# Performance work log

Hardware: AMD Instinct MI355X
Metric: run time of the kernel (lower is better)

Reference implementation:

```python
import jax, jax.numpy as jnp
import numpy as np

NR, NL, K, TOPK, C, B = 4096, 16384, 8, 10, 16, 4
W_OCC, W_MDN, W_INT = 0.2, 1.0, 0.1
LOG2PI = float(np.log(2.0 * np.pi))


def setup_inputs() -> dict:
    key = jax.random.key(0)
    ks = jax.random.split(key, 12)
    radar_indices = jnp.concatenate([
        jax.random.randint(ks[0], (NR, 1), 0, B),
        jax.random.randint(ks[1], (NR, 1), 0, 41),
        jax.random.randint(ks[2], (NR, 2), 0, 176),
    ], axis=1).astype(jnp.int32)
    lidar_indices = jnp.concatenate([
        jax.random.randint(ks[3], (NL, 1), 0, B),
        jax.random.randint(ks[4], (NL, 1), 0, 41),
        jax.random.randint(ks[5], (NL, 2), 0, 176),
    ], axis=1).astype(jnp.int32)
    return {
        'mu_off': jax.random.normal(ks[6], (NR, K, 3)) * 2.0,
        'log_sig_off': jax.random.normal(ks[7], (NR, K, 3)) * 0.3,
        'mu_int': jax.random.normal(ks[8], (NR, K, 1)),
        'occ_logit': jax.random.normal(ks[9], (NR, K, 1)),
        'mix_logit': jax.random.normal(ks[10], (NR, K, 1)),
        'lidar_features': jax.random.normal(ks[11], (NL, C)),
        'radar_indices': radar_indices,
        'lidar_indices': lidar_indices,
        'gt_topk': TOPK,
    }


def _match(radar_indices, lidar_indices, topk):
    # per-batch top-k nearest lidar voxels for each radar voxel (vectorized:
    # dense masked distance matrix replaces the per-batch python loop)
    rb, lb = radar_indices[:, 0], lidar_indices[:, 0]
    rpos = radar_indices[:, 1:].astype(jnp.float32)  # (Nr,3) zyx
    lpos = lidar_indices[:, 1:].astype(jnp.float32)  # (Nl,3)
    d2 = ((rpos * rpos).sum(-1)[:, None] + (lpos * lpos).sum(-1)[None, :]
          - 2.0 * (rpos @ lpos.T))  # (Nr,Nl) squared dist, same order as cdist
    same = rb[:, None] == lb[None, :]
    d2 = jnp.where(same, d2, jnp.inf)  # cross-batch pairs excluded
    _, nn_idx = jax.lax.top_k(-d2, topk)  # (Nr,topk) smallest distances
    matched = same.any(axis=1)  # (Nr,)
    offs_zyx = (lidar_indices[nn_idx, 1:]
                - radar_indices[:, None, 1:]).astype(jnp.float32)  # (Nr,topk,3)
    offs_zyx = jnp.where(matched[:, None, None], offs_zyx, 0.0)
    return matched, nn_idx, offs_zyx


def reference(mu_off, log_sig_off, mu_int, occ_logit, mix_logit,
              lidar_features, radar_indices, lidar_indices, gt_topk):
    matched, nn_idx, offs_zyx = _match(radar_indices, lidar_indices, gt_topk)
    gt_feat = jnp.where(matched[:, None, None], lidar_features[nn_idx], 0.0)  # (Nr,T,C)
    y = offs_zyx[..., ::-1]  # flip zyx -> xyz, (Nr,T,3)

    # occupancy BCE-with-logits against matched mask
    occ_any = occ_logit[..., 0].max(axis=1)  # (Nr,)
    tgt = matched.astype(occ_any.dtype)
    occ_loss = (tgt * jax.nn.softplus(-occ_any)
                + (1.0 - tgt) * jax.nn.softplus(occ_any)).mean()

    # MDN log-prob: (Nr,T,K) mixture components
    log_pi = jax.nn.log_softmax(mix_logit[..., 0], axis=1)  # (Nr,K)
    mu_ = mu_off[:, None, :, :]       # (Nr,1,K,3)
    ls_ = log_sig_off[:, None, :, :]
    sigma2 = jnp.exp(2.0 * ls_) + 1e-12
    y_ = y[:, :, None, :]             # (Nr,T,1,3)
    logN = -0.5 * (((y_ - mu_) ** 2) / sigma2 + 2.0 * ls_ + LOG2PI).sum(-1)  # (Nr,T,K)
    log_post = logN + log_pi[:, None, :]
    logp = jax.nn.logsumexp(log_post, axis=-1)  # (Nr,T)

    # masked means emulate boolean-index-then-mean over matched rows
    m = matched.astype(jnp.float32)
    cnt = m.sum()
    T = logp.shape[1]
    mdn_nll = -(logp * m[:, None]).sum() / (cnt * T)

    # intensity loss (C % 4 == 0 path)
    gt_int = gt_feat.reshape(gt_feat.shape[0], gt_feat.shape[1], C // 4, 4)[..., 3].mean(axis=2)  # (Nr,T)
    r = jax.nn.softmax(log_post, axis=-1)  # (Nr,T,K) responsibilities
    term = r * jnp.abs(mu_int[:, None, :, 0] - gt_int[:, :, None])  # (Nr,T,K)
    int_loss = (term * m[:, None, None]).sum() / (cnt * T * r.shape[-1])

    return W_OCC * occ_loss + W_MDN * mdn_nll + W_INT * int_loss
```

## Files before the change

kernel.cpp:

```cpp
#include <hip/hip_runtime.h>
#include <cstdint>

#define NRAD 4096
#define NLID 16384
#define KMIX 8
#define TOPK 10
#define CF   16
#define NBIN 176
#define LOG2PI 1.8378770664093453f

static constexpr unsigned INF_D2 = 62851u;

__device__ __forceinline__ void insert_key(unsigned (&t)[TOPK], unsigned key) {
#pragma unroll
    for (int i = TOPK - 1; i >= 1; --i) {
        unsigned hi = key > t[i - 1] ? key : t[i - 1];
        t[i] = hi < t[i] ? hi : t[i];
    }
    t[0] = key < t[0] ? key : t[0];
}

__device__ __forceinline__ void merge10(unsigned (&t)[TOPK], int lane,
                                        unsigned& mine, unsigned& first, unsigned& tenth) {
#pragma unroll
    for (int r = 0; r < TOPK; ++r) {
        unsigned v = t[0];
#pragma unroll
        for (int off = 32; off >= 1; off >>= 1) {
            unsigned o = __shfl_xor(v, off, 64);
            v = o < v ? o : v;
        }
        if (t[0] == v) {
#pragma unroll
            for (int i = 0; i < TOPK - 1; ++i) t[i] = t[i + 1];
            t[TOPK - 1] = 0xFFFFFFFFu;
        }
        if (lane == r) mine = v;
        if (r == 0) first = v;
        if (r == TOPK - 1) tenth = v;
    }
}

__device__ __forceinline__ float waveReduceSum(float v) {
#pragma unroll
    for (int off = 32; off >= 1; off >>= 1) v += __shfl_down(v, off, 64);
    return v;
}

__device__ __forceinline__ void scan_range(unsigned (&t)[TOPK], const uint2* __restrict__ base,
                                           int s, int e, int rz, int ry, int rx, int lane) {
    for (int i = s + lane; i < e; i += 64) {
        uint2 c = base[i];
        int dz = (int)((c.x >> 16) & 63u)  - rz;
        int dy = (int)((c.x >> 8)  & 255u) - ry;
        int dx = (int)(c.x & 255u)         - rx;
        unsigned d2 = (unsigned)(__mul24(dz, dz) + __mul24(dy, dy) + __mul24(dx, dx));
        unsigned key = (d2 << 14) | c.y;
        if (key < t[TOPK - 1]) insert_key(t, key);
    }
}

__global__ __launch_bounds__(1024) void prep_kernel(
        const int* __restrict__ lidar_indices,
        unsigned* __restrict__ packed_full,
        uint2* __restrict__ compacted,
        int* __restrict__ binoff_g,
        int* __restrict__ ctrl) {
    __shared__ int hist[NBIN];
    __shared__ int binoff_s[NBIN + 1];
    __shared__ int bcur[NBIN];
    int tid = threadIdx.x, myb = blockIdx.x;
    if (tid < NBIN) hist[tid] = 0;

    int4 li[NLID / 1024];
#pragma unroll
    for (int it = 0; it < NLID / 1024; ++it)
        li[it] = ((const int4*)lidar_indices)[it * 1024 + tid];
    __syncthreads();

#pragma unroll
    for (int it = 0; it < NLID / 1024; ++it)
        if (li[it].x == myb) atomicAdd(&hist[li[it].z], 1);
    __syncthreads();

    if (tid <= NBIN) {
        int s = 0;
        for (int j = 0; j < tid; ++j) s += hist[j];
        binoff_s[tid] = s;
    }
    __syncthreads();
    if (tid < NBIN) bcur[tid] = binoff_s[tid];
    __syncthreads();

#pragma unroll
    for (int it = 0; it < NLID / 1024; ++it) {
        int i = it * 1024 + tid;
        unsigned pos = ((unsigned)li[it].y << 16) | ((unsigned)li[it].z << 8) | (unsigned)li[it].w;
        if (li[it].x == myb) {
            packed_full[i] = ((unsigned)li[it].x << 22) | pos;
            int dst = atomicAdd(&bcur[li[it].z], 1);
            compacted[myb * NLID + dst] = make_uint2(pos, (unsigned)i);
        }
    }

    __syncthreads();
    if (tid <= NBIN) binoff_g[myb * (NBIN + 1) + tid] = binoff_s[tid];
    if (tid == 0)    ctrl[myb] = binoff_s[NBIN];
    if (myb == 0 && tid >= 64 && tid < 69) ctrl[4 + (tid - 64)] = 0;
}

__global__ __launch_bounds__(256) void topk_kernel(
        const uint2* __restrict__ compacted,
        const unsigned* __restrict__ packed_full,
        const int* __restrict__ ctrl,
        const int* __restrict__ binoff_g,
        const int* __restrict__ radar_indices,
        int* __restrict__ nn_out, int* __restrict__ matched_out) {
    int lane = threadIdx.x & 63;
    int row  = blockIdx.x * 4 + (threadIdx.x >> 6);
    int4 ri = ((const int4*)radar_indices)[row];
    int rb = ri.x, rz = ri.y, ry = ri.z, rx = ri.w;
    const int* boff = binoff_g + rb * (NBIN + 1);

    int lo = ry - 16; lo = lo < 0 ? 0 : lo;
    int hi = ry + 17; hi = hi > NBIN ? NBIN : hi;
    int s = boff[lo], e = boff[hi];

    unsigned t[TOPK];
#pragma unroll
    for (int i = 0; i < TOPK; ++i) t[i] = 0xFFFFFFFFu;

    const uint2* base = compacted + rb * NLID;
    scan_range(t, base, s, e, rz, ry, rx, lane);

    unsigned mine = 0xFFFFFFFFu, first = 0, tenth = 0;
    merge10(t, lane, mine, first, tenth);
    bool matched = true;

    unsigned lim = 0xFFFFFFFFu;
    if (lo > 0)    { unsigned d = (unsigned)(ry - lo + 1); unsigned v = d * d; lim = v < lim ? v : lim; }
    if (hi < NBIN) { unsigned d = (unsigned)(hi - ry);     unsigned v = d * d; lim = v < lim ? v : lim; }

    if ((tenth >> 14) >= lim) {
#pragma unroll
        for (int i = 0; i < TOPK; ++i) t[i] = 0xFFFFFFFFu;
        t[0] = mine;
        scan_range(t, base, boff[0], s, rz, ry, rx, lane);
        scan_range(t, base, e, boff[NBIN], rz, ry, rx, lane);
        merge10(t, lane, mine, first, tenth);
    }

    if (tenth == 0xFFFFFFFFu) {
#pragma unroll
        for (int i = 0; i < TOPK; ++i) t[i] = 0xFFFFFFFFu;
        for (int it = 0; it < NLID / 256; ++it) {
            uint4 p4 = ((const uint4*)packed_full)[it * 64 + lane];
            unsigned bse = it * 256 + lane * 4;
            unsigned ps[4] = {p4.x, p4.y, p4.z, p4.w};
#pragma unroll
            for (int j = 0; j < 4; ++j) {
                unsigned p = ps[j];
                int b  = (int)(p >> 22);
                int dz = (int)((p >> 16) & 63u)  - rz;
                int dy = (int)((p >> 8)  & 255u) - ry;
                int dx = (int)(p & 255u)         - rx;
                unsigned d2 = (unsigned)(__mul24(dz, dz) + __mul24(dy, dy) + __mul24(dx, dx));
                unsigned hi2 = (b == rb) ? d2 : INF_D2;
                insert_key(t, (hi2 << 14) | (bse + j));
            }
        }
        merge10(t, lane, mine, first, tenth);
        matched = first < (INF_D2 << 14);
    }

    if (lane < TOPK) nn_out[row * TOPK + lane] = (int)(mine & 0x3FFFu);
    if (lane == 0)   matched_out[row] = matched ? 1 : 0;
}

__global__ __launch_bounds__(256) void mdn_kernel(
        const float* __restrict__ mu_off, const float* __restrict__ log_sig_off,
        const float* __restrict__ mu_int, const float* __restrict__ occ_logit,
        const float* __restrict__ mix_logit, const float* __restrict__ lidar_features,
        const int* __restrict__ radar_indices, const int* __restrict__ lidar_indices,
        const int* __restrict__ nn, const int* __restrict__ matched,
        float* __restrict__ accum,
        unsigned* __restrict__ dctr,
        float* __restrict__ out) {
    int gid = blockIdx.x * 256 + threadIdx.x;
    int n  = gid / TOPK;
    int tt = gid - n * TOPK;
    int m  = matched[n];
    float mf = (float)m;
    int nni = nn[gid];

    int4 ri = ((const int4*)radar_indices)[n];
    int4 li = ((const int4*)lidar_indices)[nni];
    float y0 = mf * (float)(li.w - ri.w);
    float y1 = mf * (float)(li.z - ri.z);
    float y2 = mf * (float)(li.y - ri.y);

    float mix[KMIX];
    float mmax = -1e30f;
#pragma unroll
    for (int k = 0; k < KMIX; ++k) {
        mix[k] = mix_logit[n * KMIX + k];
        mmax = fmaxf(mmax, mix[k]);
    }
    float msum = 0.f;
#pragma unroll
    for (int k = 0; k < KMIX; ++k) msum += expf(mix[k] - mmax);
    float logZ = mmax + logf(msum);

    float lpost[KMIX];
    float pmax = -1e30f;
#pragma unroll
    for (int k = 0; k < KMIX; ++k) {
        int bidx = (n * KMIX + k) * 3;
        float mu0 = mu_off[bidx + 0], mu1 = mu_off[bidx + 1], mu2 = mu_off[bidx + 2];
        float l0 = log_sig_off[bidx + 0], l1 = log_sig_off[bidx + 1], l2 = log_sig_off[bidx + 2];
        float s0 = expf(2.f * l0) + 1e-12f;
        float s1 = expf(2.f * l1) + 1e-12f;
        float s2 = expf(2.f * l2) + 1e-12f;
        float d0 = y0 - mu0, d1 = y1 - mu1, d2v = y2 - mu2;
        float q = d0 * d0 / s0 + d1 * d1 / s1 + d2v * d2v / s2
                + 2.f * (l0 + l1 + l2) + 3.f * LOG2PI;
        lpost[k] = -0.5f * q + (mix[k] - logZ);
        pmax = fmaxf(pmax, lpost[k]);
    }
    float ex[KMIX];
    float se = 0.f;
#pragma unroll
    for (int k = 0; k < KMIX; ++k) { ex[k] = expf(lpost[k] - pmax); se += ex[k]; }
    float logp = pmax + logf(se);

    float gt = 0.f;
    if (m) {
        const float* lf = lidar_features + nni * CF;
        gt = 0.25f * (lf[3] + lf[7] + lf[11] + lf[15]);
    }
    float inv_se = 1.f / se;
    float isum = 0.f;
#pragma unroll
    for (int k = 0; k < KMIX; ++k)
        isum += ex[k] * inv_se * fabsf(mu_int[n * KMIX + k] - gt);

    float lp = mf * logp;
    float ip = mf * isum;
    float oc = 0.f, mc = 0.f;
    if (tt == 0) {
        float oa = -1e30f;
#pragma unroll
        for (int k = 0; k < KMIX; ++k) oa = fmaxf(oa, occ_logit[n * KMIX + k]);
        float soft_abs = log1pf(expf(-fabsf(oa)));
        oc = mf * (soft_abs + fmaxf(-oa, 0.f)) + (1.f - mf) * (soft_abs + fmaxf(oa, 0.f));
        mc = mf;
    }

    lp = waveReduceSum(lp); ip = waveReduceSum(ip);
    oc = waveReduceSum(oc); mc = waveReduceSum(mc);
    __shared__ float sA[4], sB[4], sC[4], sD[4];
    int wid = threadIdx.x >> 6, lane = threadIdx.x & 63;
    if (lane == 0) { sA[wid] = lp; sB[wid] = ip; sC[wid] = oc; sD[wid] = mc; }
    __syncthreads();
    if (threadIdx.x == 0) {
        atomicAdd(&accum[0], sA[0] + sA[1] + sA[2] + sA[3]);
        atomicAdd(&accum[1], sB[0] + sB[1] + sB[2] + sB[3]);
        atomicAdd(&accum[2], sC[0] + sC[1] + sC[2] + sC[3]);
        atomicAdd(&accum[3], sD[0] + sD[1] + sD[2] + sD[3]);
        __threadfence();
        unsigned done = atomicAdd(dctr, 1u);
        if (done == gridDim.x - 1) {
            __threadfence();
            float a = __hip_atomic_load(&accum[0], __ATOMIC_RELAXED, __HIP_MEMORY_SCOPE_AGENT);
            float b = __hip_atomic_load(&accum[1], __ATOMIC_RELAXED, __HIP_MEMORY_SCOPE_AGENT);
            float c = __hip_atomic_load(&accum[2], __ATOMIC_RELAXED, __HIP_MEMORY_SCOPE_AGENT);
            float d = __hip_atomic_load(&accum[3], __ATOMIC_RELAXED, __HIP_MEMORY_SCOPE_AGENT);
            float occ_loss = c / (float)NRAD;
            float mdn_nll  = -a / (d * (float)TOPK);
            float int_loss = b / (d * (float)TOPK * (float)KMIX);
            out[0] = 0.2f * occ_loss + mdn_nll + 0.1f * int_loss;
        }
    }
}

extern "C" void kernel_launch(void* const* d_in, const int* in_sizes, int n_in,
                              void* d_out, int out_size, void* d_ws, size_t ws_size,
                              hipStream_t stream) {
    const float* mu_off         = (const float*)d_in[0];
    const float* log_sig_off    = (const float*)d_in[1];
    const float* mu_int         = (const float*)d_in[2];
    const float* occ_logit      = (const float*)d_in[3];
    const float* mix_logit      = (const float*)d_in[4];
    const float* lidar_features = (const float*)d_in[5];
    const int*   radar_indices  = (const int*)d_in[6];
    const int*   lidar_indices  = (const int*)d_in[7];
    float* out = (float*)d_out;

    char* ws = (char*)d_ws;
    unsigned* packed_full = (unsigned*)(ws + 0);
    uint2*    compacted   = (uint2*)(ws + 65536);
    int*      ctrl        = (int*)(ws + 589824);
    int*      nn          = (int*)(ws + 589888);
    int*      matched     = (int*)(ws + 753728);
    int*      binoff_g    = (int*)(ws + 770112);

    float*    accum = (float*)(ctrl + 4);
    unsigned* dctr  = (unsigned*)(ctrl + 8);

    hipLaunchKernelGGL(prep_kernel, dim3(4), dim3(1024), 0, stream,
                       lidar_indices, packed_full, compacted, binoff_g, ctrl);
    hipLaunchKernelGGL(topk_kernel, dim3(NRAD / 4), dim3(256), 0, stream,
                       compacted, packed_full, ctrl, binoff_g, radar_indices, nn, matched);
    hipLaunchKernelGGL(mdn_kernel, dim3(NRAD * TOPK / 256), dim3(256), 0, stream,
                       mu_off, log_sig_off, mu_int, occ_logit, mix_logit,
                       lidar_features, radar_indices, lidar_indices,
                       nn, matched, accum, dctr, out);
}
```

Measured before the change: 112.5 us.

## Narrow y-window, vectorize candidate scan with prefetch, parallel bin prefix scan

The y-bin search window in the top-k kernel shrinks from ±16 to ±13 bins, so fewer lidar candidates are scanned before the exactness check, which still falls back to a full scan when needed. The first-pass scan now reads two candidates per lane with 16-byte loads and prefetches the next chunk so load latency overlaps compute. The serial per-thread prefix sum over histogram bins becomes a wavefront shuffle scan, and the unused ctrl count is dropped. A narrower window may trigger the fallback full scan more often.

```diff
diff --git a/kernel.cpp b/kernel.cpp
--- a/kernel.cpp
+++ b/kernel.cpp
@@ -7,6 +7,7 @@
 #define TOPK 10
 #define CF   16
 #define NBIN 176
+#define YWIN 13
 #define LOG2PI 1.8378770664093453f
 
 static constexpr unsigned INF_D2 = 62851u;
@@ -83,10 +84,22 @@
         if (li[it].x == myb) atomicAdd(&hist[li[it].z], 1);
     __syncthreads();
 
-    if (tid <= NBIN) {
-        int s = 0;
-        for (int j = 0; j < tid; ++j) s += hist[j];
-        binoff_s[tid] = s;
+    if (tid < 64) {
+        int carry = 0;
+#pragma unroll
+        for (int c = 0; c < 3; ++c) {
+            int idx = c * 64 + tid;
+            int h = (idx < NBIN) ? hist[idx] : 0;
+            int v = h;
+#pragma unroll
+            for (int off = 1; off < 64; off <<= 1) {
+                int u = __shfl_up(v, off, 64);
+                if (tid >= off) v += u;
+            }
+            if (idx < NBIN) binoff_s[idx] = carry + v - h;
+            carry += __shfl(v, 63, 64);
+        }
+        if (tid == 0) binoff_s[NBIN] = carry;
     }
     __syncthreads();
     if (tid < NBIN) bcur[tid] = binoff_s[tid];
@@ -105,14 +118,12 @@
 
     __syncthreads();
     if (tid <= NBIN) binoff_g[myb * (NBIN + 1) + tid] = binoff_s[tid];
-    if (tid == 0)    ctrl[myb] = binoff_s[NBIN];
     if (myb == 0 && tid >= 64 && tid < 69) ctrl[4 + (tid - 64)] = 0;
 }
 
 __global__ __launch_bounds__(256) void topk_kernel(
         const uint2* __restrict__ compacted,
         const unsigned* __restrict__ packed_full,
-        const int* __restrict__ ctrl,
         const int* __restrict__ binoff_g,
         const int* __restrict__ radar_indices,
         int* __restrict__ nn_out, int* __restrict__ matched_out) {
@@ -122,8 +133,8 @@
     int rb = ri.x, rz = ri.y, ry = ri.z, rx = ri.w;
     const int* boff = binoff_g + rb * (NBIN + 1);
 
-    int lo = ry - 16; lo = lo < 0 ? 0 : lo;
-    int hi = ry + 17; hi = hi > NBIN ? NBIN : hi;
+    int lo = ry - YWIN;      lo = lo < 0 ? 0 : lo;
+    int hi = ry + YWIN + 1;  hi = hi > NBIN ? NBIN : hi;
     int s = boff[lo], e = boff[hi];
 
     unsigned t[TOPK];
@@ -131,7 +142,32 @@
     for (int i = 0; i < TOPK; ++i) t[i] = 0xFFFFFFFFu;
 
     const uint2* base = compacted + rb * NLID;
-    scan_range(t, base, s, e, rz, ry, rx, lane);
+    int s0 = s & ~1;
+    const uint4* src4 = (const uint4*)(base + s0);
+    int iters = (e - s0 + 127) >> 7;
+    uint4 q = src4[lane];
+    for (int it = 0; it < iters; ++it) {
+        uint4 qn = q;
+        if (it + 1 < iters) qn = src4[(it + 1) * 64 + lane];
+        int p = s0 + (it * 64 + lane) * 2;
+        {
+            int dz = (int)((q.x >> 16) & 63u)  - rz;
+            int dy = (int)((q.x >> 8)  & 255u) - ry;
+            int dx = (int)(q.x & 255u)         - rx;
+            unsigned d2 = (unsigned)(__mul24(dz, dz) + __mul24(dy, dy) + __mul24(dx, dx));
+            unsigned key = (p >= s && p < e) ? ((d2 << 14) | q.y) : 0xFFFFFFFFu;
+            if (key < t[TOPK - 1]) insert_key(t, key);
+        }
+        {
+            int dz = (int)((q.z >> 16) & 63u)  - rz;
+            int dy = (int)((q.z >> 8)  & 255u) - ry;
+            int dx = (int)(q.z & 255u)         - rx;
+            unsigned d2 = (unsigned)(__mul24(dz, dz) + __mul24(dy, dy) + __mul24(dx, dx));
+            unsigned key = (p + 1 < e) ? ((d2 << 14) | q.w) : 0xFFFFFFFFu;
+            if (key < t[TOPK - 1]) insert_key(t, key);
+        }
+        q = qn;
+    }
 
     unsigned mine = 0xFFFFFFFFu, first = 0, tenth = 0;
     merge10(t, lane, mine, first, tenth);
@@ -310,7 +346,7 @@
     hipLaunchKernelGGL(prep_kernel, dim3(4), dim3(1024), 0, stream,
                        lidar_indices, packed_full, compacted, binoff_g, ctrl);
     hipLaunchKernelGGL(topk_kernel, dim3(NRAD / 4), dim3(256), 0, stream,
-                       compacted, packed_full, ctrl, binoff_g, radar_indices, nn, matched);
+                       compacted, packed_full, binoff_g, radar_indices, nn, matched);
     hipLaunchKernelGGL(mdn_kernel, dim3(NRAD * TOPK / 256), dim3(256), 0, stream,
                        mu_off, log_sig_off, mu_int, occ_logit, mix_logit,
                        lidar_features, radar_indices, lidar_indices,
```

Result: no change. 112.6 us (+0.1%).
